# Kernel optimization log

Measured on AMD Instinct MI355X. Metric: run time of the kernel, lower is better.

Reference implementation:

```python
import jax, jax.numpy as jnp
import numpy as np

B, N, DIM, K, H, R = 128, 196, 384, 16, 6, 4  # batch, tokens, channels, bases, heads, adapter ratio


def setup_inputs() -> dict:
    key = jax.random.key(0)
    ks = jax.random.split(key, 4)
    d_r = DIM // R
    return {
        "x": jax.random.normal(ks[0], (B, N, DIM), jnp.float32),
        "W1": jax.random.normal(ks[1], (DIM, d_r), jnp.float32) * 0.02,
        "b1": jnp.zeros((d_r,), jnp.float32),
        "W2": jax.random.normal(ks[2], (d_r, K * H), jnp.float32) * 0.02,
        "b2": jnp.zeros((K * H,), jnp.float32),
        "weight_bank": jax.random.normal(ks[3], (K, N, N), jnp.float32) * 0.02,
    }


def reference(x, W1, b1, W2, b2, weight_bank):
    Bsz, n, C = x.shape
    hdim = C // H
    # adapter MLP: Linear -> GELU(exact/erf, torch default) -> Linear
    hid = jax.nn.gelu(x @ W1 + b1, approximate=False)
    mix = (hid @ W2 + b2).reshape(Bsz, n, K, H)
    # mode='softmax': normalize mixing policy over the k bases
    mix = jax.nn.softmax(mix, axis=2)
    # dynamic per-sample token-mixing matrix [B, n, n, H]
    weight = jnp.einsum('bnkh,knm->bnmh', mix, weight_bank)
    # mix tokens: contract over source token index n
    xh = x.reshape(Bsz, n, H, hdim)
    out = jnp.einsum('bnhc,bnmh->bmhc', xh, weight).reshape(Bsz, n, C)
    return out
```

## Files before the change

kernel.cpp:

```cpp
#include <hip/hip_runtime.h>
#include <math.h>

#define BB  128
#define NN  196
#define CDIM 384
#define KK  16
#define HH  6
#define DR  96
#define HD  64
#define MP  208
#define NCHUNK 7
#define PLANE 6656

typedef __attribute__((ext_vector_type(8))) short bf16x8;
typedef __attribute__((ext_vector_type(4))) float f32x4;

__device__ __forceinline__ unsigned short f2bf(float f) {
    unsigned u = __float_as_uint(f);
    u += 0x7FFFu + ((u >> 16) & 1u);
    return (unsigned short)(u >> 16);
}
__device__ __forceinline__ unsigned pk2bf(float lo, float hi) {
    return (unsigned)f2bf(lo) | ((unsigned)f2bf(hi) << 16);
}

union AFrag { unsigned u[4]; bf16x8 f; };

__global__ __launch_bounds__(256) void prep_kernel(
    const float* __restrict__ W1, const float* __restrict__ W2,
    const float* __restrict__ wb,
    unsigned short* __restrict__ W1T, unsigned short* __restrict__ W2T,
    unsigned short* __restrict__ wbT)
{
    const int bid = blockIdx.x;
    const int t   = threadIdx.x;
    if (bid < DR) {
        const int c = bid;
        for (int k = t; k < CDIM; k += 256)
            W1T[(size_t)c * CDIM + k] = f2bf(W1[(size_t)k * DR + c]);
        if (t < DR)
            W2T[(size_t)c * DR + t] = f2bf(W2[(size_t)t * DR + c]);
    } else {
        const int n = bid - DR;
        const int m = t;
        if (m < MP) {
            unsigned o[8] = {0u, 0u, 0u, 0u, 0u, 0u, 0u, 0u};
            if (n < NN && m < NN) {
                #pragma unroll
                for (int j = 0; j < 8; ++j) {
                    const float a = wb[((size_t)(2 * j)     * NN + n) * NN + m];
                    const float c = wb[((size_t)(2 * j + 1) * NN + n) * NN + m];
                    o[j] = pk2bf(a, c);
                }
            }
            unsigned* dst = (unsigned*)(wbT + ((size_t)n * MP + m) * KK);
            *(uint4*)dst       = make_uint4(o[0], o[1], o[2], o[3]);
            *(uint4*)(dst + 4) = make_uint4(o[4], o[5], o[6], o[7]);
        }
    }
}

__global__ __launch_bounds__(256, 3) void mixa_kernel(
    const float* __restrict__ x,  const unsigned short* __restrict__ W1T,
    const float* __restrict__ b1, const unsigned short* __restrict__ W2T,
    const float* __restrict__ b2, const unsigned short* __restrict__ wbT,
    unsigned short* __restrict__ A)
{
    __shared__ unsigned short hidb[32][104];
    __shared__ unsigned short msc[32][96];

    const int t    = threadIdx.x;
    const int w    = t >> 6;
    const int wm   = w & 1;
    const int wc   = w >> 1;
    const int lane = t & 63;
    const int l15  = lane & 15;
    const int lq   = lane >> 4;
    const int b    = blockIdx.x & 127;
    const int nc   = blockIdx.x >> 7;
    const int n0   = nc * 32;

    f32x4 acc[3];
    #pragma unroll
    for (int ct = 0; ct < 3; ++ct) {
        const float bj = b1[wc * 48 + ct * 16 + l15];
        acc[ct] = (f32x4){bj, bj, bj, bj};
    }
    const int nrow = n0 + wm * 16 + l15;
    const bool rv  = (nrow < NN);
    const float* xrow = x + ((size_t)b * NN + nrow) * CDIM;
    float4 u = make_float4(0.f, 0.f, 0.f, 0.f);
    float4 v = make_float4(0.f, 0.f, 0.f, 0.f);
    if (rv) {
        u = *(const float4*)(xrow + 8 * lq);
        v = *(const float4*)(xrow + 8 * lq + 4);
    }
    for (int kc = 0; kc < CDIM; kc += 32) {
        float4 un = make_float4(0.f, 0.f, 0.f, 0.f);
        float4 vn = make_float4(0.f, 0.f, 0.f, 0.f);
        if (rv && kc + 32 < CDIM) {
            un = *(const float4*)(xrow + kc + 32 + 8 * lq);
            vn = *(const float4*)(xrow + kc + 32 + 8 * lq + 4);
        }
        AFrag af;
        af.u[0] = pk2bf(u.x, u.y); af.u[1] = pk2bf(u.z, u.w);
        af.u[2] = pk2bf(v.x, v.y); af.u[3] = pk2bf(v.z, v.w);
        #pragma unroll
        for (int ct = 0; ct < 3; ++ct) {
            const bf16x8 bf = *(const bf16x8*)(W1T + (size_t)(wc * 48 + ct * 16 + l15) * CDIM + kc + 8 * lq);
            acc[ct] = __builtin_amdgcn_mfma_f32_16x16x32_bf16(af.f, bf, acc[ct], 0, 0, 0);
        }
        u = un; v = vn;
    }
    #pragma unroll
    for (int ct = 0; ct < 3; ++ct)
        #pragma unroll
        for (int r = 0; r < 4; ++r) {
            const float vv = acc[ct][r];
            hidb[wm * 16 + lq * 4 + r][wc * 48 + ct * 16 + l15] =
                f2bf(0.5f * vv * (1.0f + erff(vv * 0.70710678118654752f)));
        }
    __syncthreads();

    f32x4 acc2[3];
    #pragma unroll
    for (int ct = 0; ct < 3; ++ct) {
        const float bj = b2[wc * 48 + ct * 16 + l15];
        acc2[ct] = (f32x4){bj, bj, bj, bj};
    }
    #pragma unroll
    for (int kc = 0; kc < DR; kc += 32) {
        const bf16x8 af = *(const bf16x8*)&hidb[wm * 16 + l15][kc + 8 * lq];
        #pragma unroll
        for (int ct = 0; ct < 3; ++ct) {
            const bf16x8 bf = *(const bf16x8*)(W2T + (size_t)(wc * 48 + ct * 16 + l15) * DR + kc + 8 * lq);
            acc2[ct] = __builtin_amdgcn_mfma_f32_16x16x32_bf16(af, bf, acc2[ct], 0, 0, 0);
        }
    }
    __syncthreads();

    #pragma unroll
    for (int ct = 0; ct < 3; ++ct)
        #pragma unroll
        for (int r = 0; r < 4; ++r)
            hidb[wm * 16 + lq * 4 + r][wc * 48 + ct * 16 + l15] = f2bf(acc2[ct][r]);
    __syncthreads();

    if (t < 192) {
        const int r = t / 6, h = t - r * 6;
        float lg[KK];
        float mx = -1e30f;
        #pragma unroll
        for (int k = 0; k < KK; ++k) {
            lg[k] = __uint_as_float((unsigned)hidb[r][6 * k + h] << 16);
            mx = fmaxf(mx, lg[k]);
        }
        float s = 0.f;
        #pragma unroll
        for (int k = 0; k < KK; ++k) { lg[k] = __expf(lg[k] - mx); s += lg[k]; }
        const float inv = 1.0f / s;
        unsigned o[8];
        #pragma unroll
        for (int jj = 0; jj < 8; ++jj)
            o[jj] = pk2bf(lg[2 * jj] * inv, lg[2 * jj + 1] * inv);
        unsigned* op = (unsigned*)&msc[r][16 * h];
        *(uint4*)op       = make_uint4(o[0], o[1], o[2], o[3]);
        *(uint4*)(op + 4) = make_uint4(o[4], o[5], o[6], o[7]);
    }
    __syncthreads();

    const bf16x8 z8 = {0, 0, 0, 0, 0, 0, 0, 0};
    const f32x4  cz = {0.f, 0.f, 0.f, 0.f};
    const size_t bc6 = ((size_t)b * NCHUNK + nc) * HH;
    const bool kv = (lq < 2);
    const bool hv = (l15 < HH);

    bf16x8 ta[13], tb[13];
    {
        const unsigned short* wp = wbT + ((size_t)(n0 + w) * MP + l15) * KK + 8 * lq;
        #pragma unroll
        for (int mt = 0; mt < 13; ++mt)
            ta[mt] = kv ? *(const bf16x8*)(wp + (size_t)(mt * 16) * KK) : z8;
    }

    #pragma unroll
    for (int ii = 0; ii < 4; ++ii) {
        {
            const int nl = 8 * ii + w;
            const bf16x8 bmix = (hv && kv)
                ? *(const bf16x8*)&msc[nl][l15 * 16 + 8 * lq] : z8;
            {
                const unsigned short* wp = wbT + ((size_t)(n0 + nl + 4) * MP + l15) * KK + 8 * lq;
                #pragma unroll
                for (int mt = 0; mt < 13; ++mt)
                    tb[mt] = kv ? *(const bf16x8*)(wp + (size_t)(mt * 16) * KK) : z8;
            }
            unsigned short* p0 = A + (bc6 + l15) * PLANE + (size_t)nl * MP + lq * 4;
            #pragma unroll
            for (int mt = 0; mt < 13; ++mt) {
                const f32x4 c = __builtin_amdgcn_mfma_f32_16x16x32_bf16(ta[mt], bmix, cz, 0, 0, 0);
                if (hv) {
                    *(uint2*)(p0 + mt * 16) =
                        make_uint2(pk2bf(c[0], c[1]), pk2bf(c[2], c[3]));
                }
            }
        }
        {
            const int nl = 8 * ii + w + 4;
            const bf16x8 bmix = (hv && kv)
                ? *(const bf16x8*)&msc[nl][l15 * 16 + 8 * lq] : z8;
            if (ii < 3) {
                const unsigned short* wp = wbT + ((size_t)(n0 + nl + 4) * MP + l15) * KK + 8 * lq;
                #pragma unroll
                for (int mt = 0; mt < 13; ++mt)
                    ta[mt] = kv ? *(const bf16x8*)(wp + (size_t)(mt * 16) * KK) : z8;
            }
            unsigned short* p0 = A + (bc6 + l15) * PLANE + (size_t)nl * MP + lq * 4;
            #pragma unroll
            for (int mt = 0; mt < 13; ++mt) {
                const f32x4 c = __builtin_amdgcn_mfma_f32_16x16x32_bf16(tb[mt], bmix, cz, 0, 0, 0);
                if (hv) {
                    *(uint2*)(p0 + mt * 16) =
                        make_uint2(pk2bf(c[0], c[1]), pk2bf(c[2], c[3]));
                }
            }
        }
    }
}

__global__ __launch_bounds__(192, 3) void mix_gemm_kernel(
    const float* __restrict__ x, const unsigned short* __restrict__ Ab,
    float* __restrict__ out)
{
    __shared__ unsigned short xT[192][40];
    __shared__ unsigned short As[3][32][68];

    const int t    = threadIdx.x;
    const int bid  = blockIdx.x;
    const int b    = bid & 127;
    const int sub  = bid >> 7;
    const int q    = sub >> 1;
    const int hp   = sub & 1;
    const int m0   = q * 52;
    const int qvalid = (q == 3) ? 40 : 52;
    const int lw   = t >> 6;
    const int hbase = hp * 3;
    const int lane = t & 63;
    const int l15  = lane & 15;
    const int lq   = lane >> 4;
    const int c0   = hp * 192;

    const f32x4 cz = {0.f, 0.f, 0.f, 0.f};
    f32x4 acc[4][4];
    #pragma unroll
    for (int mt = 0; mt < 4; ++mt)
        #pragma unroll
        for (int ct = 0; ct < 4; ++ct) acc[mt][ct] = cz;

    unsigned long long av[8];

    {
        const size_t bc6 = (size_t)b * NCHUNK * HH + hbase;
        #pragma unroll
        for (int i = 0; i < 8; ++i) {
            const int P = t + 192 * i;
            const int row = P >> 4, p = P & 15;
            av[i] = *(const unsigned long long*)(
                Ab + (bc6 + (size_t)(row >> 5)) * PLANE + (size_t)(row & 31) * MP + m0 + 4 * p);
        }
    }

    for (int nc = 0; nc < NCHUNK; ++nc) {
        const int n0 = nc * 32;
        if (nc) __syncthreads();

        #pragma unroll
        for (int i = 0; i < 8; ++i) {
            const int P = t + 192 * i;
            const int row = P >> 4, p = P & 15;
            *(unsigned long long*)&As[row >> 5][row & 31][4 * p] = av[i];
        }

        #pragma unroll
        for (int it = 0; it < 4; ++it) {
            const int task = t + 192 * it;
            const int p  = task & 15;
            const int cq = task >> 4;
            const int n  = n0 + 2 * p;
            float4 va = make_float4(0.f, 0.f, 0.f, 0.f);
            float4 vb = make_float4(0.f, 0.f, 0.f, 0.f);
            if (n < NN)     va = *(const float4*)(x + ((size_t)b * NN + n) * CDIM + c0 + 4 * cq);
            if (n + 1 < NN) vb = *(const float4*)(x + ((size_t)b * NN + n + 1) * CDIM + c0 + 4 * cq);
            *(unsigned*)&xT[4 * cq + 0][2 * p] = pk2bf(va.x, vb.x);
            *(unsigned*)&xT[4 * cq + 1][2 * p] = pk2bf(va.y, vb.y);
            *(unsigned*)&xT[4 * cq + 2][2 * p] = pk2bf(va.z, vb.z);
            *(unsigned*)&xT[4 * cq + 3][2 * p] = pk2bf(va.w, vb.w);
        }
        __syncthreads();

        if (nc + 1 < NCHUNK) {
            const size_t bc6 = ((size_t)b * NCHUNK + nc + 1) * HH + hbase;
            #pragma unroll
            for (int i = 0; i < 8; ++i) {
                const int P = t + 192 * i;
                const int row = P >> 4, p = P & 15;
                av[i] = *(const unsigned long long*)(
                    Ab + (bc6 + (size_t)(row >> 5)) * PLANE + (size_t)(row & 31) * MP + m0 + 4 * p);
            }
        }

        bf16x8 afr[4], bfr[4];
        #pragma unroll
        for (int mt = 0; mt < 4; ++mt) {
            union { unsigned short s[8]; bf16x8 v; } u;
            #pragma unroll
            for (int j = 0; j < 8; ++j)
                u.s[j] = As[lw][8 * lq + j][mt * 16 + l15];
            afr[mt] = u.v;
        }
        #pragma unroll
        for (int ct = 0; ct < 4; ++ct)
            bfr[ct] = *(const bf16x8*)&xT[lw * 64 + ct * 16 + l15][8 * lq];
        #pragma unroll
        for (int mt = 0; mt < 4; ++mt)
            #pragma unroll
            for (int ct = 0; ct < 4; ++ct)
                acc[mt][ct] = __builtin_amdgcn_mfma_f32_16x16x32_bf16(
                    afr[mt], bfr[ct], acc[mt][ct], 0, 0, 0);
    }

    const int h = hbase + lw;
    #pragma unroll
    for (int mt = 0; mt < 4; ++mt) {
        #pragma unroll
        for (int r = 0; r < 4; ++r) {
            const int ms = mt * 16 + lq * 4 + r;
            if (ms < qvalid) {
                float* op = out + ((size_t)b * NN + m0 + ms) * CDIM + h * HD + l15;
                #pragma unroll
                for (int ct = 0; ct < 4; ++ct)
                    op[ct * 16] = acc[mt][ct][r];
            }
        }
    }
}

__global__ __launch_bounds__(128, 3) void adapter_kernel(
    const float* __restrict__ x,   const unsigned short* __restrict__ W1T,
    const float* __restrict__ b1,  const unsigned short* __restrict__ W2T,
    const float* __restrict__ b2,  unsigned short* __restrict__ mix_out)
{
    __shared__ unsigned short hidb[16][104];

    const int t    = threadIdx.x;
    const int wc   = t >> 6;
    const int lane = t & 63;
    const int l15  = lane & 15;
    const int lq   = lane >> 4;
    const int row0 = blockIdx.x * 16;

    f32x4 acc[3];
    #pragma unroll
    for (int ct = 0; ct < 3; ++ct) {
        const float bj = b1[wc * 48 + ct * 16 + l15];
        acc[ct] = (f32x4){bj, bj, bj, bj};
    }
    const float* xrow = x + (size_t)(row0 + l15) * CDIM;
    for (int kc = 0; kc < CDIM; kc += 32) {
        const float4 u = *(const float4*)(xrow + kc + 8 * lq);
        const float4 v = *(const float4*)(xrow + kc + 8 * lq + 4);
        AFrag af;
        af.u[0] = pk2bf(u.x, u.y); af.u[1] = pk2bf(u.z, u.w);
        af.u[2] = pk2bf(v.x, v.y); af.u[3] = pk2bf(v.z, v.w);
        #pragma unroll
        for (int ct = 0; ct < 3; ++ct) {
            const bf16x8 bf = *(const bf16x8*)(W1T + (size_t)(wc * 48 + ct * 16 + l15) * CDIM + kc + 8 * lq);
            acc[ct] = __builtin_amdgcn_mfma_f32_16x16x32_bf16(af.f, bf, acc[ct], 0, 0, 0);
        }
    }
    #pragma unroll
    for (int ct = 0; ct < 3; ++ct)
        #pragma unroll
        for (int r = 0; r < 4; ++r) {
            const float vv = acc[ct][r];
            hidb[lq * 4 + r][wc * 48 + ct * 16 + l15] =
                f2bf(0.5f * vv * (1.0f + erff(vv * 0.70710678118654752f)));
        }
    __syncthreads();

    f32x4 acc2[3];
    #pragma unroll
    for (int ct = 0; ct < 3; ++ct) {
        const float bj = b2[wc * 48 + ct * 16 + l15];
        acc2[ct] = (f32x4){bj, bj, bj, bj};
    }
    #pragma unroll
    for (int kc = 0; kc < DR; kc += 32) {
        const bf16x8 af = *(const bf16x8*)&hidb[l15][kc + 8 * lq];
        #pragma unroll
        for (int ct = 0; ct < 3; ++ct) {
            const bf16x8 bf = *(const bf16x8*)(W2T + (size_t)(wc * 48 + ct * 16 + l15) * DR + kc + 8 * lq);
            acc2[ct] = __builtin_amdgcn_mfma_f32_16x16x32_bf16(af, bf, acc2[ct], 0, 0, 0);
        }
    }
    __syncthreads();

    #pragma unroll
    for (int ct = 0; ct < 3; ++ct)
        #pragma unroll
        for (int r = 0; r < 4; ++r)
            hidb[lq * 4 + r][wc * 48 + ct * 16 + l15] = f2bf(acc2[ct][r]);
    __syncthreads();

    if (t < 96) {
        const int r = t / 6, h = t % 6;
        float lg[KK];
        float mx = -1e30f;
        #pragma unroll
        for (int k = 0; k < KK; ++k) {
            lg[k] = __uint_as_float((unsigned)hidb[r][6 * k + h] << 16);
            mx = fmaxf(mx, lg[k]);
        }
        float s = 0.f;
        #pragma unroll
        for (int k = 0; k < KK; ++k) { lg[k] = __expf(lg[k] - mx); s += lg[k]; }
        const float inv = 1.0f / s;
        unsigned o[8];
        #pragma unroll
        for (int jj = 0; jj < 8; ++jj)
            o[jj] = pk2bf(lg[2 * jj] * inv, lg[2 * jj + 1] * inv);
        unsigned* op = (unsigned*)(mix_out + ((size_t)(row0 + r) * HH + h) * KK);
        *(uint4*)op       = make_uint4(o[0], o[1], o[2], o[3]);
        *(uint4*)(op + 4) = make_uint4(o[4], o[5], o[6], o[7]);
    }
}

__global__ __launch_bounds__(192, 3) void mix_mfma_fb_kernel(
    const float* __restrict__ x,  const unsigned short* __restrict__ mixb,
    const unsigned short* __restrict__ wbT, float* __restrict__ out)
{
    __shared__ unsigned short xT[192][40];
    __shared__ unsigned short Asb[3][64][40];

    const int t    = threadIdx.x;
    const int bid  = blockIdx.x;
    const int b    = bid & 127;
    const int sub  = bid >> 7;
    const int q    = sub >> 1;
    const int hp   = sub & 1;
    const int m0   = q * 52;
    const int qvalid = (q == 3) ? 40 : 52;
    const int lw   = t >> 6;
    const int hbase = hp * 3;
    const int lane = t & 63;
    const int l15  = lane & 15;
    const int lq   = lane >> 4;
    const int c0   = hp * 192;

    const bf16x8 z8 = {0, 0, 0, 0, 0, 0, 0, 0};
    const f32x4  cz = {0.f, 0.f, 0.f, 0.f};

    f32x4 acc[4][4];
    #pragma unroll
    for (int mt = 0; mt < 4; ++mt)
        #pragma unroll
        for (int ct = 0; ct < 4; ++ct) acc[mt][ct] = cz;

    for (int nc = 0; nc < 7; ++nc) {
        const int n0 = nc * 32;
        __syncthreads();

        #pragma unroll
        for (int it = 0; it < 4; ++it) {
            const int task = t + 192 * it;
            const int p  = task & 15;
            const int cq = task >> 4;
            const int n  = n0 + 2 * p;
            float4 va = make_float4(0.f, 0.f, 0.f, 0.f);
            float4 vb = make_float4(0.f, 0.f, 0.f, 0.f);
            if (n < NN)     va = *(const float4*)(x + ((size_t)b * NN + n) * CDIM + c0 + 4 * cq);
            if (n + 1 < NN) vb = *(const float4*)(x + ((size_t)b * NN + n + 1) * CDIM + c0 + 4 * cq);
            *(unsigned*)&xT[4 * cq + 0][2 * p] = pk2bf(va.x, vb.x);
            *(unsigned*)&xT[4 * cq + 1][2 * p] = pk2bf(va.y, vb.y);
            *(unsigned*)&xT[4 * cq + 2][2 * p] = pk2bf(va.z, vb.z);
            *(unsigned*)&xT[4 * cq + 3][2 * p] = pk2bf(va.w, vb.w);
        }

        for (int nl = lw; nl < 32; nl += 3) {
            const int n = n0 + nl;
            if (n < NN) {
                bf16x8 af = z8;
                if (l15 < HH && lq < 2)
                    af = *(const bf16x8*)(mixb + (((size_t)b * NN + n) * HH + l15) * KK + 8 * lq);
                #pragma unroll
                for (int mt = 0; mt < 4; ++mt) {
                    const int m = m0 + mt * 16 + l15;
                    bf16x8 bf = z8;
                    if (lq < 2 && m < NN)
                        bf = *(const bf16x8*)(wbT + ((size_t)n * MP + m) * KK + 8 * lq);
                    const f32x4 c = __builtin_amdgcn_mfma_f32_16x16x32_bf16(af, bf, cz, 0, 0, 0);
                    #pragma unroll
                    for (int r = 0; r < 4; ++r) {
                        const int hh = lq * 4 + r;
                        if (hh >= hbase && hh < hbase + 3)
                            Asb[hh - hbase][mt * 16 + l15][nl] = f2bf(c[r]);
                    }
                }
            } else {
                #pragma unroll
                for (int mt = 0; mt < 4; ++mt)
                    #pragma unroll
                    for (int r = 0; r < 4; ++r) {
                        const int hh = lq * 4 + r;
                        if (hh >= hbase && hh < hbase + 3)
                            Asb[hh - hbase][mt * 16 + l15][nl] = 0;
                    }
            }
        }
        __syncthreads();

        bf16x8 afr[4], bfr[4];
        #pragma unroll
        for (int mt = 0; mt < 4; ++mt)
            afr[mt] = *(const bf16x8*)&Asb[lw][mt * 16 + l15][8 * lq];
        #pragma unroll
        for (int ct = 0; ct < 4; ++ct)
            bfr[ct] = *(const bf16x8*)&xT[lw * 64 + ct * 16 + l15][8 * lq];
        #pragma unroll
        for (int mt = 0; mt < 4; ++mt)
            #pragma unroll
            for (int ct = 0; ct < 4; ++ct)
                acc[mt][ct] = __builtin_amdgcn_mfma_f32_16x16x32_bf16(
                    afr[mt], bfr[ct], acc[mt][ct], 0, 0, 0);
    }

    const int h = hbase + lw;
    #pragma unroll
    for (int mt = 0; mt < 4; ++mt) {
        #pragma unroll
        for (int r = 0; r < 4; ++r) {
            const int ms = mt * 16 + lq * 4 + r;
            if (ms < qvalid) {
                float* op = out + ((size_t)b * NN + m0 + ms) * CDIM + h * HD + l15;
                #pragma unroll
                for (int ct = 0; ct < 4; ++ct)
                    op[ct * 16] = acc[mt][ct][r];
            }
        }
    }
}

extern "C" void kernel_launch(void* const* d_in, const int* in_sizes, int n_in,
                              void* d_out, int out_size, void* d_ws, size_t ws_size,
                              hipStream_t stream) {
    (void)in_sizes; (void)n_in; (void)out_size;
    const float* x  = (const float*)d_in[0];
    const float* W1 = (const float*)d_in[1];
    const float* b1 = (const float*)d_in[2];
    const float* W2 = (const float*)d_in[3];
    const float* b2 = (const float*)d_in[4];
    const float* wb = (const float*)d_in[5];
    float* out = (float*)d_out;

    const size_t W1T_OFF  = 0;
    const size_t W2T_OFF  = 73728;
    const size_t WBT_OFF  = 92160;
    const size_t A_OFF    = 1583104;
    const size_t NEED     = A_OFF + 71565312ull + 1024ull;

    unsigned short* w1t = (unsigned short*)((char*)d_ws + W1T_OFF);
    unsigned short* w2t = (unsigned short*)((char*)d_ws + W2T_OFF);
    unsigned short* wbt = (unsigned short*)((char*)d_ws + WBT_OFF);

    prep_kernel<<<DR + 224, 256, 0, stream>>>(W1, W2, wb, w1t, w2t, wbt);

    if (ws_size >= NEED) {
        unsigned short* Ab = (unsigned short*)((char*)d_ws + A_OFF);
        mixa_kernel<<<BB * NCHUNK, 256, 0, stream>>>(x, w1t, b1, w2t, b2, wbt, Ab);
        mix_gemm_kernel<<<8 * BB, 192, 0, stream>>>(x, Ab, out);
    } else {
        unsigned short* mixbuf = (unsigned short*)((char*)d_ws + A_OFF);
        adapter_kernel<<<(BB * NN) / 16, 128, 0, stream>>>(x, w1t, b1, w2t, b2, mixbuf);
        mix_mfma_fb_kernel<<<8 * BB, 192, 0, stream>>>(x, mixbuf, wbt, out);
    }
}
```

Baseline: 191.8 us.

## Stage weight-bank slab through double-buffered LDS in mixa_kernel

Replaces the per-wave register prefetch of 13 bf16x8 weight-bank tiles (half the lanes idle) with cooperative, fully coalesced uint4 loads of two token rows at a time into a double-buffered LDS tile. Each wave then computes half of the m-tiles for one row, and occupancy is raised to 4 blocks per SM. A sched_barrier is added in mix_gemm_kernel to pin the instruction order of its prefetch, and the A workspace offset is shifted. The change adds a __syncthreads per row iteration and more LDS use, which may limit the intended occupancy gain.

```diff
diff --git a/kernel.cpp b/kernel.cpp
--- a/kernel.cpp
+++ b/kernel.cpp
@@ -60,7 +60,7 @@
     }
 }
 
-__global__ __launch_bounds__(256, 3) void mixa_kernel(
+__global__ __launch_bounds__(256, 4) void mixa_kernel(
     const float* __restrict__ x,  const unsigned short* __restrict__ W1T,
     const float* __restrict__ b1, const unsigned short* __restrict__ W2T,
     const float* __restrict__ b2, const unsigned short* __restrict__ wbT,
@@ -68,6 +68,8 @@
 {
     __shared__ unsigned short hidb[32][104];
     __shared__ unsigned short msc[32][96];
+    __shared__ unsigned short wbuf[2][2][208][16];
+    __shared__ uint4 wslack[1];
 
     const int t    = threadIdx.x;
     const int w    = t >> 6;
@@ -80,6 +82,16 @@
     const int nc   = blockIdx.x >> 7;
     const int n0   = nc * 32;
 
+    const unsigned short* slab = wbT + (size_t)n0 * (MP * KK);
+    uint4 av0, av1, av2, av3;
+    {
+        const uint4* sp = (const uint4*)slab;
+        av0 = sp[t];
+        av1 = sp[t + 256];
+        av2 = sp[t + 512];
+        av3 = (t < 64) ? sp[t + 768] : make_uint4(0u, 0u, 0u, 0u);
+    }
+
     f32x4 acc[3];
     #pragma unroll
     for (int ct = 0; ct < 3; ++ct) {
@@ -172,60 +184,55 @@
     const bf16x8 z8 = {0, 0, 0, 0, 0, 0, 0, 0};
     const f32x4  cz = {0.f, 0.f, 0.f, 0.f};
     const size_t bc6 = ((size_t)b * NCHUNK + nc) * HH;
-    const bool kv = (lq < 2);
-    const bool hv = (l15 < HH);
-
-    bf16x8 ta[13], tb[13];
-    {
-        const unsigned short* wp = wbT + ((size_t)(n0 + w) * MP + l15) * KK + 8 * lq;
-        #pragma unroll
-        for (int mt = 0; mt < 13; ++mt)
-            ta[mt] = kv ? *(const bf16x8*)(wp + (size_t)(mt * 16) * KK) : z8;
-    }
-
-    #pragma unroll
-    for (int ii = 0; ii < 4; ++ii) {
+    const int  rw  = w >> 1;
+    const int  mh  = w & 1;
+    const bool hv  = (l15 < HH);
+    const bool kv  = (lq < 2);
+
+    for (int r = 0; r < 16; ++r) {
+        if (r) __syncthreads();
         {
-            const int nl = 8 * ii + w;
-            const bf16x8 bmix = (hv && kv)
-                ? *(const bf16x8*)&msc[nl][l15 * 16 + 8 * lq] : z8;
-            {
-                const unsigned short* wp = wbT + ((size_t)(n0 + nl + 4) * MP + l15) * KK + 8 * lq;
-                #pragma unroll
-                for (int mt = 0; mt < 13; ++mt)
-                    tb[mt] = kv ? *(const bf16x8*)(wp + (size_t)(mt * 16) * KK) : z8;
-            }
-            unsigned short* p0 = A + (bc6 + l15) * PLANE + (size_t)nl * MP + lq * 4;
+            uint4* dp = (uint4*)&wbuf[r & 1][0][0][0];
+            dp[t]       = av0;
+            dp[t + 256] = av1;
+            dp[t + 512] = av2;
+            if (t < 64) dp[t + 768] = av3;
+        }
+        if (r + 1 < 16) {
+            const uint4* sp = (const uint4*)slab + (size_t)(r + 1) * 832;
+            av0 = sp[t];
+            av1 = sp[t + 256];
+            av2 = sp[t + 512];
+            if (t < 64) av3 = sp[t + 768];
+        }
+        __syncthreads();
+
+        const int nl = 2 * r + rw;
+        const bf16x8 bmix = (hv && kv)
+            ? *(const bf16x8*)&msc[nl][l15 * 16 + 8 * lq] : z8;
+        const unsigned short* wrow = &wbuf[r & 1][rw][0][0];
+        unsigned short* p0 = A + (bc6 + l15) * PLANE + (size_t)nl * MP + lq * 4;
+        if (mh == 0) {
             #pragma unroll
-            for (int mt = 0; mt < 13; ++mt) {
-                const f32x4 c = __builtin_amdgcn_mfma_f32_16x16x32_bf16(ta[mt], bmix, cz, 0, 0, 0);
-                if (hv) {
+            for (int mt = 0; mt < 7; ++mt) {
+                const bf16x8 afr = *(const bf16x8*)(wrow + (mt * 16 + l15) * 16 + 8 * lq);
+                const f32x4 c = __builtin_amdgcn_mfma_f32_16x16x32_bf16(afr, bmix, cz, 0, 0, 0);
+                if (hv)
                     *(uint2*)(p0 + mt * 16) =
                         make_uint2(pk2bf(c[0], c[1]), pk2bf(c[2], c[3]));
-                }
-            }
-        }
-        {
-            const int nl = 8 * ii + w + 4;
-            const bf16x8 bmix = (hv && kv)
-                ? *(const bf16x8*)&msc[nl][l15 * 16 + 8 * lq] : z8;
-            if (ii < 3) {
-                const unsigned short* wp = wbT + ((size_t)(n0 + nl + 4) * MP + l15) * KK + 8 * lq;
-                #pragma unroll
-                for (int mt = 0; mt < 13; ++mt)
-                    ta[mt] = kv ? *(const bf16x8*)(wp + (size_t)(mt * 16) * KK) : z8;
-            }
-            unsigned short* p0 = A + (bc6 + l15) * PLANE + (size_t)nl * MP + lq * 4;
+            }
+        } else {
             #pragma unroll
-            for (int mt = 0; mt < 13; ++mt) {
-                const f32x4 c = __builtin_amdgcn_mfma_f32_16x16x32_bf16(tb[mt], bmix, cz, 0, 0, 0);
-                if (hv) {
+            for (int mt = 7; mt < 13; ++mt) {
+                const bf16x8 afr = *(const bf16x8*)(wrow + (mt * 16 + l15) * 16 + 8 * lq);
+                const f32x4 c = __builtin_amdgcn_mfma_f32_16x16x32_bf16(afr, bmix, cz, 0, 0, 0);
+                if (hv)
                     *(uint2*)(p0 + mt * 16) =
                         make_uint2(pk2bf(c[0], c[1]), pk2bf(c[2], c[3]));
-                }
-            }
-        }
-    }
+            }
+        }
+    }
+    (void)wslack;
 }
 
 __global__ __launch_bounds__(192, 3) void mix_gemm_kernel(
@@ -308,6 +315,7 @@
                     Ab + (bc6 + (size_t)(row >> 5)) * PLANE + (size_t)(row & 31) * MP + m0 + 4 * p);
             }
         }
+        __builtin_amdgcn_sched_barrier(0);
 
         bf16x8 afr[4], bfr[4];
         #pragma unroll
@@ -565,7 +573,7 @@
     const size_t W1T_OFF  = 0;
     const size_t W2T_OFF  = 73728;
     const size_t WBT_OFF  = 92160;
-    const size_t A_OFF    = 1583104;
+    const size_t A_OFF    = 1584128;
     const size_t NEED     = A_OFF + 71565312ull + 1024ull;
 
     unsigned short* w1t = (unsigned short*)((char*)d_ws + W1T_OFF);
```

Result: no change. 192.2 us (+0.2%).
